# Optimization experiments

Hardware: AMD Instinct MI355X
Metric: run time of the kernel (lower is better)

The kernel has to match this reference:

```python
import jax, jax.numpy as jnp
import numpy as np

B, N, E = 64, 256, 2048          # graphs per batch, nodes per subgraph, edges per subgraph
V, D, H = 50000, 128, 4          # vocab_size, hidden_dim, heads
NEG_SLOPE = 0.2                  # PyG GATConv default LeakyReLU slope


def setup_inputs() -> dict:
    key = jax.random.key(0)
    ks = jax.random.split(key, 16)
    s = 0.05
    return {
        "neighbors_node1": jax.random.randint(ks[0], (B, N), 0, V),
        "neighbors_node2": jax.random.randint(ks[1], (B, N), 0, V),
        "adj1": jax.random.randint(ks[2], (B, 2, E), 0, N),
        "adj2": jax.random.randint(ks[3], (B, 2, E), 0, N),
        "emb": jax.random.normal(ks[4], (V + 1, D), jnp.float32) * 0.02,
        # GATConv 1: lin weight [H*D, D], att_src/att_dst [H, D], bias [D] (concat=False)
        "W1": jax.random.normal(ks[5], (H * D, D), jnp.float32) * s,
        "att_src1": jax.random.normal(ks[6], (H, D), jnp.float32) * s,
        "att_dst1": jax.random.normal(ks[7], (H, D), jnp.float32) * s,
        "b1": jnp.zeros((D,), jnp.float32),
        # GATConv 2
        "W2": jax.random.normal(ks[8], (H * D, D), jnp.float32) * s,
        "att_src2": jax.random.normal(ks[9], (H, D), jnp.float32) * s,
        "att_dst2": jax.random.normal(ks[10], (H, D), jnp.float32) * s,
        "b2": jnp.zeros((D,), jnp.float32),
        # final MLP: Linear(2D -> 1)
        "mlp_w": jax.random.normal(ks[11], (1, 2 * D), jnp.float32) * s,
        "mlp_b": jnp.zeros((1,), jnp.float32),
    }


def _gat_conv(x, edge_index, W, a_src, a_dst, bias):
    """PyG GATConv, concat=False (mean over heads), with self-loops.
    x: [N, D] node features; edge_index: [2, E] (row=src j, col=dst i)."""
    xh = (x @ W.T).reshape(N, H, D)                      # [N, H, D]
    loop = jnp.arange(N)
    src = jnp.concatenate([edge_index[0], loop])          # [E+N]
    dst = jnp.concatenate([edge_index[1], loop])
    asrc = jnp.einsum('nhd,hd->nh', xh, a_src)            # [N, H]
    adst = jnp.einsum('nhd,hd->nh', xh, a_dst)
    e = jax.nn.leaky_relu(asrc[src] + adst[dst], NEG_SLOPE)   # [E+N, H]
    # softmax over incoming edges of each dst node
    m = jax.ops.segment_max(e, dst, num_segments=N)
    ex = jnp.exp(e - m[dst])
    denom = jax.ops.segment_sum(ex, dst, num_segments=N)
    alpha = ex / denom[dst]                               # [E+N, H]
    out = jax.ops.segment_sum(xh[src] * alpha[:, :, None], dst, num_segments=N)  # [N, H, D]
    return out.mean(axis=1) + bias                        # [N, D]


def reference(neighbors_node1, neighbors_node2, adj1, adj2, emb,
              W1, att_src1, att_dst1, b1,
              W2, att_src2, att_dst2, b2,
              mlp_w, mlp_b):
    f1 = jax.vmap(lambda n, ei: _gat_conv(emb[n], ei, W1, att_src1, att_dst1, b1))(
        neighbors_node1, adj1)                            # [B, N, D]
    f2 = jax.vmap(lambda n, ei: _gat_conv(emb[n], ei, W2, att_src2, att_dst2, b2))(
        neighbors_node2, adj2)
    feats = jnp.concatenate([f1[:, 0], f2[:, 0]], axis=-1)  # center node of each subgraph -> [B, 2D]
    return (feats @ mlp_w.T + mlp_b)[:, 0]                # [B]
```

## Files before the change

### kernel.cpp

```cpp
#include <hip/hip_runtime.h>
#include <hip/hip_bf16.h>

#define Bg 64
#define Nn 256
#define Ee 2048
#define Dd 128
#define Hh 4
#define MAXJ 40
#define RS 132
#define MAGIC 0x9E3779B1u

__device__ __forceinline__ float bf2f(unsigned short u) {
    return __uint_as_float(((unsigned)u) << 16);
}

__global__ __launch_bounds__(512) void gat_fused_kernel(
    const int* nn1, const int* nn2, const int* adj1, const int* adj2,
    const void* emb,
    const void* W1, const void* as1, const void* ad1, const void* b1,
    const void* W2, const void* as2, const void* ad2, const void* b2,
    const void* mlpw, const void* mlpb,
    float* wv, int f32arg, void* out)
{
    __shared__ float s_wv[24 * RS];
    __shared__ float s_rows[2 * MAXJ * RS];
    __shared__ int   s_nodes[2][Nn];
    __shared__ int   s_srcj[2][MAXJ];
    __shared__ int   s_gid[2 * MAXJ];
    __shared__ int   s_cnt[2];
    __shared__ int   s_f32;
    __shared__ float s_ps[2 * MAXJ * Hh], s_pm[2 * MAXJ * Hh];
    __shared__ float s_pd[2 * Hh], s_hval[2 * Hh], s_bdot[2];
    __shared__ float s_red[2];

    const int tid = threadIdx.x;
    const int x = blockIdx.x;

    if (x < 8) {
        const int l = x >> 2, h = x & 3;
        float* s_av   = s_wv;
        float* s_part = s_rows;

        int f32 = f32arg;
        if (f32 < 0) {
            if (tid < 64) {
                float v = bf2f(((const unsigned short*)W1)[tid]);
                unsigned long long m = __ballot(!(v > -64.f && v < 64.f));
                if (tid == 0) s_f32 = (m != 0ull) ? 1 : 0;
            }
            __syncthreads();
            f32 = s_f32;
        }

        if (tid < 384) {
            int t = tid >> 7, d = tid & 127;
            const void* p; long off;
            if (t == 0)      { p = l ? as2 : as1; off = (long)h * Dd + d; }
            else if (t == 1) { p = l ? ad2 : ad1; off = (long)h * Dd + d; }
            else             { p = mlpw;          off = (long)l * Dd + d; }
            s_av[tid] = f32 ? ((const float*)p)[off]
                            : bf2f(((const unsigned short*)p)[off]);
        }
        __syncthreads();

        {
            const int kc = (tid & 31) * 4;
            const int dg = tid >> 5;
            const int d0 = dg * 8;
            float acc[3][4] = {};
            if (f32) {
                const float* Wf = (const float*)(l ? W2 : W1) + (long)h * Dd * Dd;
                #pragma unroll
                for (int dd = 0; dd < 8; ++dd) {
                    int d = d0 + dd;
                    float4 w = *(const float4*)(Wf + (long)d * Dd + kc);
                    #pragma unroll
                    for (int t = 0; t < 3; ++t) {
                        float a = s_av[t * Dd + d];
                        acc[t][0] += a * w.x; acc[t][1] += a * w.y;
                        acc[t][2] += a * w.z; acc[t][3] += a * w.w;
                    }
                }
            } else {
                const unsigned short* Wb =
                    (const unsigned short*)(l ? W2 : W1) + (long)h * Dd * Dd;
                #pragma unroll
                for (int dd = 0; dd < 8; ++dd) {
                    int d = d0 + dd;
                    ushort4 u = *(const ushort4*)(Wb + (long)d * Dd + kc);
                    float wx = bf2f(u.x), wy = bf2f(u.y);
                    float wz = bf2f(u.z), ww = bf2f(u.w);
                    #pragma unroll
                    for (int t = 0; t < 3; ++t) {
                        float a = s_av[t * Dd + d];
                        acc[t][0] += a * wx; acc[t][1] += a * wy;
                        acc[t][2] += a * wz; acc[t][3] += a * ww;
                    }
                }
            }
            const int dg2 = tid >> 5;
            #pragma unroll
            for (int t = 0; t < 3; ++t)
                *(float4*)&s_part[(dg2 * 3 + t) * Dd + kc] =
                    make_float4(acc[t][0], acc[t][1], acc[t][2], acc[t][3]);
        }
        __syncthreads();

        if (tid < 384) {
            int t = tid >> 7, k = tid & 127;
            float s = 0.f;
            #pragma unroll
            for (int g = 0; g < 16; ++g) s += s_part[(g * 3 + t) * Dd + k];
            wv[((l * 3 + t) * 4 + h) * Dd + k] = s;
        }

        if (h == 0) {
            float p = 0.f;
            if (tid < 128) {
                const void* bias = l ? b2 : b1;
                float bv = f32 ? ((const float*)bias)[tid]
                               : bf2f(((const unsigned short*)bias)[tid]);
                p = bv * s_av[2 * Dd + tid];
            }
            #pragma unroll
            for (int off = 32; off > 0; off >>= 1) p += __shfl_down(p, off);
            if (tid == 0 || tid == 64) s_red[tid >> 6] = p;
            __syncthreads();
            if (tid == 0) {
                float a = s_red[0] + s_red[1];
                if (l == 0) a += f32 ? ((const float*)mlpb)[0]
                                     : bf2f(((const unsigned short*)mlpb)[0]);
                wv[3072 + l] = a;
            }
        }

        __threadfence();
        __syncthreads();
        if (tid == 0)
            atomicExch((unsigned*)wv + 3080 + x, MAGIC);
        return;
    }

    const int b = x - 8;

    const int* adjp0 = adj1 + (long)b * 2 * Ee;
    const int* adjp1 = adj2 + (long)b * 2 * Ee;
    int4 d0 = ((const int4*)(adjp0 + Ee))[tid];
    int4 s0 = ((const int4*)adjp0)[tid];
    int4 d1 = ((const int4*)(adjp1 + Ee))[tid];
    int4 s1 = ((const int4*)adjp1)[tid];

    {
        int l = tid >> 8, n = tid & 255;
        s_nodes[l][n] = (l ? nn2 : nn1)[b * Nn + n];
    }
    if (tid < 2) s_cnt[tid] = 0;

    int f32 = f32arg;
    if (f32 < 0 && tid < 64) {
        float v = bf2f(((const unsigned short*)W1)[tid]);
        unsigned long long m = __ballot(!(v > -64.f && v < 64.f));
        if (tid == 0) s_f32 = (m != 0ull) ? 1 : 0;
    }
    __syncthreads();
    if (f32 < 0) f32 = s_f32;

    {
        #define SCAN1(c, sv, l) \
            if ((c) == 0) { int p = atomicAdd(&s_cnt[l], 1); \
                            if (p < MAXJ - 1) s_srcj[l][p] = (sv); }
        SCAN1(d0.x, s0.x, 0) SCAN1(d0.y, s0.y, 0)
        SCAN1(d0.z, s0.z, 0) SCAN1(d0.w, s0.w, 0)
        SCAN1(d1.x, s1.x, 1) SCAN1(d1.y, s1.y, 1)
        SCAN1(d1.z, s1.z, 1) SCAN1(d1.w, s1.w, 1)
        #undef SCAN1
    }
    __syncthreads();

    int c0 = s_cnt[0]; if (c0 > MAXJ - 1) c0 = MAXJ - 1; c0 += 1;
    int c1 = s_cnt[1]; if (c1 > MAXJ - 1) c1 = MAXJ - 1; c1 += 1;
    const int tot = c0 + c1;

    if (tid < 2 * MAXJ) {
        int l = tid >= MAXJ;
        int j = l ? tid - MAXJ : tid;
        int cl = l ? c1 : c0;
        int base = l ? c0 : 0;
        if (j < cl) {
            int src = (j == cl - 1) ? 0 : s_srcj[l][j];
            s_gid[base + j] = s_nodes[l][src];
        }
    }
    __syncthreads();

    if (f32) {
        for (int idx = tid; idx < tot * 32; idx += 512) {
            int j = idx >> 5, k4 = (idx & 31) << 2;
            long gid = s_gid[j];
            float4 f = ((const float4*)emb)[gid * 32 + (k4 >> 2)];
            *(float4*)&s_rows[j * RS + k4] = f;
        }
    } else {
        for (int idx = tid; idx < tot * 16; idx += 512) {
            int j = idx >> 4, k8 = (idx & 15) << 3;
            long gid = s_gid[j];
            uint4 u = *(const uint4*)((const unsigned short*)emb + gid * Dd + k8);
            float4 f0 = make_float4(bf2f(u.x & 0xffff), bf2f(u.x >> 16),
                                    bf2f(u.y & 0xffff), bf2f(u.y >> 16));
            float4 f1 = make_float4(bf2f(u.z & 0xffff), bf2f(u.z >> 16),
                                    bf2f(u.w & 0xffff), bf2f(u.w >> 16));
            *(float4*)&s_rows[j * RS + k8] = f0;
            *(float4*)&s_rows[j * RS + k8 + 4] = f1;
        }
    }

    if (tid < 8) {
        unsigned* fl = (unsigned*)wv + 3080 + tid;
        while (atomicAdd(fl, 0u) != MAGIC) __builtin_amdgcn_s_sleep(2);
    }
    __syncthreads();
    __threadfence();

    for (int i = tid; i < 768; i += 512) {
        float4 f = ((const float4*)wv)[i];
        int el = i * 4, row = el >> 7, k = el & 127;
        *(float4*)&s_wv[row * RS + k] = f;
    }
    if (tid < 2) s_bdot[tid] = wv[3072 + tid];
    __syncthreads();

    const int ntask = tot * 8 + 8;
    for (int task = tid; task < ntask; task += 512) {
        int j, h, t, l;
        if (task < tot * 8) {
            j = task >> 3; h = (task >> 1) & 3; t = (task & 1) ? 2 : 0;
            l = (j < c0) ? 0 : 1;
        } else {
            int z = task - tot * 8;
            l = z >> 2; h = z & 3; t = 1;
            j = l ? (tot - 1) : (c0 - 1);
        }
        const float4* r4 = (const float4*)(s_rows + j * RS);
        const float4* w4 = (const float4*)(s_wv + ((l * 3 + t) * Hh + h) * RS);
        float acc = 0.f;
        #pragma unroll 8
        for (int k = 0; k < 32; ++k) {
            float4 a = r4[k], w = w4[k];
            acc += a.x * w.x + a.y * w.y + a.z * w.z + a.w * w.w;
        }
        if (task < tot * 8) {
            if (task & 1) s_pm[j * Hh + h] = acc;
            else          s_ps[j * Hh + h] = acc;
        } else {
            s_pd[(l << 2) | h] = acc;
        }
    }
    __syncthreads();

    {
        const int w = tid >> 6, lane = tid & 63;
        const int l = w >> 2, h = w & 3;
        const int j0 = l ? c0 : 0;
        const int cntl = (l ? tot : c0) - j0;
        const float pd = s_pd[w];
        const bool valid = lane < cntl;
        const int j = j0 + (valid ? lane : 0);
        float e = valid ? (s_ps[j * Hh + h] + pd) : -1e30f;
        e = (e >= 0.f) ? e : 0.2f * e;
        float m = e;
        #pragma unroll
        for (int off = 32; off > 0; off >>= 1)
            m = fmaxf(m, __shfl_xor(m, off));
        float ex = valid ? expf(e - m) : 0.f;
        float pm = valid ? s_pm[j * Hh + h] : 0.f;
        float den = ex, num = ex * pm;
        #pragma unroll
        for (int off = 32; off > 0; off >>= 1) {
            den += __shfl_xor(den, off);
            num += __shfl_xor(num, off);
        }
        if (lane == 0) s_hval[w] = num / den;
    }
    __syncthreads();

    if (tid == 0) {
        float r = 0.25f * (s_hval[0] + s_hval[1] + s_hval[2] + s_hval[3]) + s_bdot[0]
                + 0.25f * (s_hval[4] + s_hval[5] + s_hval[6] + s_hval[7]) + s_bdot[1];
        if (f32) ((float*)out)[b] = r;
        else     ((__hip_bfloat16*)out)[b] = __float2bfloat16(r);
    }
}

extern "C" void kernel_launch(void* const* d_in, const int* in_sizes, int n_in,
                              void* d_out, int out_size, void* d_ws, size_t ws_size,
                              hipStream_t stream) {
    float* wv = (float*)d_ws;

    int sz5 = (in_sizes && n_in > 5) ? in_sizes[5] : 0;
    int f32arg = (sz5 == 512 * 128 * 4) ? 1 : ((sz5 == 512 * 128 * 2) ? 0 : -1);

    gat_fused_kernel<<<8 + Bg, 512, 0, stream>>>(
        (const int*)d_in[0],
        (const int*)d_in[1],
        (const int*)d_in[2],
        (const int*)d_in[3],
        d_in[4],
        d_in[5],   d_in[6],   d_in[7],
        d_in[8],
        d_in[9],   d_in[10],  d_in[11],
        d_in[12],
        d_in[13],  d_in[14],
        wv, f32arg, d_out);
}
```

Before: 111.5 us.

## Replicate weight-vector precompute per block, drop inter-block flag wait

```diff
diff --git a/kernel.cpp b/kernel.cpp
--- a/kernel.cpp
+++ b/kernel.cpp
@@ -8,7 +8,6 @@
 #define Hh 4
 #define MAXJ 40
 #define RS 132
-#define MAGIC 0x9E3779B1u
 
 __device__ __forceinline__ float bf2f(unsigned short u) {
     return __uint_as_float(((unsigned)u) << 16);
@@ -19,129 +18,22 @@
     const void* emb,
     const void* W1, const void* as1, const void* ad1, const void* b1,
     const void* W2, const void* as2, const void* ad2, const void* b2,
-    const void* mlpw, const void* mlpb,
-    float* wv, int f32arg, void* out)
+    const void* mlpw, const void* mlpb, int f32arg, void* out)
 {
     __shared__ float s_wv[24 * RS];
     __shared__ float s_rows[2 * MAXJ * RS];
+    __shared__ float s_att[2304];
     __shared__ int   s_nodes[2][Nn];
     __shared__ int   s_srcj[2][MAXJ];
     __shared__ int   s_gid[2 * MAXJ];
     __shared__ int   s_cnt[2];
     __shared__ int   s_f32;
     __shared__ float s_ps[2 * MAXJ * Hh], s_pm[2 * MAXJ * Hh];
-    __shared__ float s_pd[2 * Hh], s_hval[2 * Hh], s_bdot[2];
-    __shared__ float s_red[2];
+    __shared__ float s_pd[8], s_hval[8];
+    __shared__ float s_red[4];
 
     const int tid = threadIdx.x;
-    const int x = blockIdx.x;
-
-    if (x < 8) {
-        const int l = x >> 2, h = x & 3;
-        float* s_av   = s_wv;
-        float* s_part = s_rows;
-
-        int f32 = f32arg;
-        if (f32 < 0) {
-            if (tid < 64) {
-                float v = bf2f(((const unsigned short*)W1)[tid]);
-                unsigned long long m = __ballot(!(v > -64.f && v < 64.f));
-                if (tid == 0) s_f32 = (m != 0ull) ? 1 : 0;
-            }
-            __syncthreads();
-            f32 = s_f32;
-        }
-
-        if (tid < 384) {
-            int t = tid >> 7, d = tid & 127;
-            const void* p; long off;
-            if (t == 0)      { p = l ? as2 : as1; off = (long)h * Dd + d; }
-            else if (t == 1) { p = l ? ad2 : ad1; off = (long)h * Dd + d; }
-            else             { p = mlpw;          off = (long)l * Dd + d; }
-            s_av[tid] = f32 ? ((const float*)p)[off]
-                            : bf2f(((const unsigned short*)p)[off]);
-        }
-        __syncthreads();
-
-        {
-            const int kc = (tid & 31) * 4;
-            const int dg = tid >> 5;
-            const int d0 = dg * 8;
-            float acc[3][4] = {};
-            if (f32) {
-                const float* Wf = (const float*)(l ? W2 : W1) + (long)h * Dd * Dd;
-                #pragma unroll
-                for (int dd = 0; dd < 8; ++dd) {
-                    int d = d0 + dd;
-                    float4 w = *(const float4*)(Wf + (long)d * Dd + kc);
-                    #pragma unroll
-                    for (int t = 0; t < 3; ++t) {
-                        float a = s_av[t * Dd + d];
-                        acc[t][0] += a * w.x; acc[t][1] += a * w.y;
-                        acc[t][2] += a * w.z; acc[t][3] += a * w.w;
-                    }
-                }
-            } else {
-                const unsigned short* Wb =
-                    (const unsigned short*)(l ? W2 : W1) + (long)h * Dd * Dd;
-                #pragma unroll
-                for (int dd = 0; dd < 8; ++dd) {
-                    int d = d0 + dd;
-                    ushort4 u = *(const ushort4*)(Wb + (long)d * Dd + kc);
-                    float wx = bf2f(u.x), wy = bf2f(u.y);
-                    float wz = bf2f(u.z), ww = bf2f(u.w);
-                    #pragma unroll
-                    for (int t = 0; t < 3; ++t) {
-                        float a = s_av[t * Dd + d];
-                        acc[t][0] += a * wx; acc[t][1] += a * wy;
-                        acc[t][2] += a * wz; acc[t][3] += a * ww;
-                    }
-                }
-            }
-            const int dg2 = tid >> 5;
-            #pragma unroll
-            for (int t = 0; t < 3; ++t)
-                *(float4*)&s_part[(dg2 * 3 + t) * Dd + kc] =
-                    make_float4(acc[t][0], acc[t][1], acc[t][2], acc[t][3]);
-        }
-        __syncthreads();
-
-        if (tid < 384) {
-            int t = tid >> 7, k = tid & 127;
-            float s = 0.f;
-            #pragma unroll
-            for (int g = 0; g < 16; ++g) s += s_part[(g * 3 + t) * Dd + k];
-            wv[((l * 3 + t) * 4 + h) * Dd + k] = s;
-        }
-
-        if (h == 0) {
-            float p = 0.f;
-            if (tid < 128) {
-                const void* bias = l ? b2 : b1;
-                float bv = f32 ? ((const float*)bias)[tid]
-                               : bf2f(((const unsigned short*)bias)[tid]);
-                p = bv * s_av[2 * Dd + tid];
-            }
-            #pragma unroll
-            for (int off = 32; off > 0; off >>= 1) p += __shfl_down(p, off);
-            if (tid == 0 || tid == 64) s_red[tid >> 6] = p;
-            __syncthreads();
-            if (tid == 0) {
-                float a = s_red[0] + s_red[1];
-                if (l == 0) a += f32 ? ((const float*)mlpb)[0]
-                                     : bf2f(((const unsigned short*)mlpb)[0]);
-                wv[3072 + l] = a;
-            }
-        }
-
-        __threadfence();
-        __syncthreads();
-        if (tid == 0)
-            atomicExch((unsigned*)wv + 3080 + x, MAGIC);
-        return;
-    }
-
-    const int b = x - 8;
+    const int b = blockIdx.x;
 
     const int* adjp0 = adj1 + (long)b * 2 * Ee;
     const int* adjp1 = adj2 + (long)b * 2 * Ee;
@@ -157,13 +49,61 @@
     if (tid < 2) s_cnt[tid] = 0;
 
     int f32 = f32arg;
-    if (f32 < 0 && tid < 64) {
-        float v = bf2f(((const unsigned short*)W1)[tid]);
-        unsigned long long m = __ballot(!(v > -64.f && v < 64.f));
-        if (tid == 0) s_f32 = (m != 0ull) ? 1 : 0;
-    }
-    __syncthreads();
-    if (f32 < 0) f32 = s_f32;
+    if (f32 < 0) {
+        if (tid < 64) {
+            float v = bf2f(((const unsigned short*)W1)[tid]);
+            unsigned long long m = __ballot(!(v > -64.f && v < 64.f));
+            if (tid == 0) s_f32 = (m != 0ull) ? 1 : 0;
+        }
+        __syncthreads();
+        f32 = s_f32;
+    }
+
+    if (f32) {
+        for (int i = tid; i < 576; i += 512) {
+            int e = i * 4;
+            const float* p; int dst;
+            if (e < 2048) {
+                int l = e >> 10, t = (e >> 9) & 1, h = (e >> 7) & 3, d = e & 127;
+                p = (const float*)(l ? (t ? ad2 : as2) : (t ? ad1 : as1)) + h * Dd + d;
+                dst = ((l * 2 + t) * 4 + h) * Dd + d;
+            } else {
+                p = (const float*)mlpw + (e - 2048);
+                dst = e;
+            }
+            *(float4*)&s_att[dst] = *(const float4*)p;
+        }
+    } else {
+        if (tid < 288) {
+            int e = tid * 8;
+            const unsigned short* p; int dst;
+            if (e < 2048) {
+                int l = e >> 10, t = (e >> 9) & 1, h = (e >> 7) & 3, d = e & 127;
+                p = (const unsigned short*)(l ? (t ? ad2 : as2) : (t ? ad1 : as1)) + h * Dd + d;
+                dst = ((l * 2 + t) * 4 + h) * Dd + d;
+            } else {
+                p = (const unsigned short*)mlpw + (e - 2048);
+                dst = e;
+            }
+            uint4 u = *(const uint4*)p;
+            *(float4*)&s_att[dst] = make_float4(bf2f(u.x & 0xffff), bf2f(u.x >> 16),
+                                                bf2f(u.y & 0xffff), bf2f(u.y >> 16));
+            *(float4*)&s_att[dst + 4] = make_float4(bf2f(u.z & 0xffff), bf2f(u.z >> 16),
+                                                    bf2f(u.w & 0xffff), bf2f(u.w >> 16));
+        }
+    }
+
+    float bv = 0.f;
+    if (tid < 256) {
+        int l = tid >> 7, d = tid & 127;
+        const void* bp = l ? b2 : b1;
+        bv = f32 ? ((const float*)bp)[d] : bf2f(((const unsigned short*)bp)[d]);
+    }
+    float mb = 0.f;
+    if (tid == 0)
+        mb = f32 ? ((const float*)mlpb)[0] : bf2f(((const unsigned short*)mlpb)[0]);
+
+    __syncthreads();
 
     {
         #define SCAN1(c, sv, l) \
@@ -193,40 +133,146 @@
     }
     __syncthreads();
 
+    const int na = f32 ? tot * 32 : tot * 16;
+    float4 ga, gb; uint4 ua;
+    bool va = false, vb = false;
     if (f32) {
-        for (int idx = tid; idx < tot * 32; idx += 512) {
+        if (tid < na) {
+            int j = tid >> 5, k4 = (tid & 31) << 2;
+            ga = ((const float4*)emb)[(long)s_gid[j] * 32 + (k4 >> 2)];
+            va = true;
+        }
+        int t2 = tid + 512;
+        if (t2 < na) {
+            int j = t2 >> 5, k4 = (t2 & 31) << 2;
+            gb = ((const float4*)emb)[(long)s_gid[j] * 32 + (k4 >> 2)];
+            vb = true;
+        }
+    } else {
+        if (tid < na) {
+            int j = tid >> 4, k8 = (tid & 15) << 3;
+            ua = *(const uint4*)((const unsigned short*)emb + (long)s_gid[j] * Dd + k8);
+            va = true;
+        }
+    }
+
+    {
+        const int w = tid >> 6, lane = tid & 63;
+        const int l = w >> 2, h = w & 3;
+        const float* a0 = s_att + ((l * 2 + 0) * 4 + h) * Dd;
+        const float* a1 = s_att + ((l * 2 + 1) * 4 + h) * Dd;
+        const float* a2 = s_att + 2048 + l * Dd;
+        if (f32) {
+            const int k0 = (lane & 31) * 4;
+            const int d0f = (lane >> 5) * 64;
+            const float* Wf = (const float*)(l ? W2 : W1) + h * Dd * Dd;
+            float acc[3][4] = {};
+            #pragma unroll 8
+            for (int i = 0; i < 64; ++i) {
+                int d = d0f + i;
+                float4 wr = *(const float4*)(Wf + d * Dd + k0);
+                float x0 = a0[d], x1 = a1[d], x2 = a2[d];
+                acc[0][0] += x0 * wr.x; acc[0][1] += x0 * wr.y;
+                acc[0][2] += x0 * wr.z; acc[0][3] += x0 * wr.w;
+                acc[1][0] += x1 * wr.x; acc[1][1] += x1 * wr.y;
+                acc[1][2] += x1 * wr.z; acc[1][3] += x1 * wr.w;
+                acc[2][0] += x2 * wr.x; acc[2][1] += x2 * wr.y;
+                acc[2][2] += x2 * wr.z; acc[2][3] += x2 * wr.w;
+            }
+            #pragma unroll
+            for (int t = 0; t < 3; ++t)
+                #pragma unroll
+                for (int c = 0; c < 4; ++c)
+                    acc[t][c] += __shfl_xor(acc[t][c], 32);
+            if (lane < 32) {
+                #pragma unroll
+                for (int t = 0; t < 3; ++t)
+                    *(float4*)&s_wv[((l * 3 + t) * 4 + h) * RS + k0] =
+                        make_float4(acc[t][0], acc[t][1], acc[t][2], acc[t][3]);
+            }
+        } else {
+            const int k0 = (lane & 15) * 8;
+            const int d0b = (lane >> 4) * 32;
+            const unsigned short* Wb =
+                (const unsigned short*)(l ? W2 : W1) + h * Dd * Dd;
+            float acc[3][8] = {};
+            #pragma unroll 4
+            for (int i = 0; i < 32; ++i) {
+                int d = d0b + i;
+                uint4 u = *(const uint4*)(Wb + d * Dd + k0);
+                float wc[8] = { bf2f(u.x & 0xffff), bf2f(u.x >> 16),
+                                bf2f(u.y & 0xffff), bf2f(u.y >> 16),
+                                bf2f(u.z & 0xffff), bf2f(u.z >> 16),
+                                bf2f(u.w & 0xffff), bf2f(u.w >> 16) };
+                float x0 = a0[d], x1 = a1[d], x2 = a2[d];
+                #pragma unroll
+                for (int c = 0; c < 8; ++c) {
+                    acc[0][c] += x0 * wc[c];
+                    acc[1][c] += x1 * wc[c];
+                    acc[2][c] += x2 * wc[c];
+                }
+            }
+            #pragma unroll
+            for (int t = 0; t < 3; ++t)
+                #pragma unroll
+                for (int c = 0; c < 8; ++c) {
+                    acc[t][c] += __shfl_xor(acc[t][c], 16);
+                    acc[t][c] += __shfl_xor(acc[t][c], 32);
+                }
+            if (lane < 16) {
+                #pragma unroll
+                for (int t = 0; t < 3; ++t) {
+                    *(float4*)&s_wv[((l * 3 + t) * 4 + h) * RS + k0] =
+                        make_float4(acc[t][0], acc[t][1], acc[t][2], acc[t][3]);
+                    *(float4*)&s_wv[((l * 3 + t) * 4 + h) * RS + k0 + 4] =
+                        make_float4(acc[t][4], acc[t][5], acc[t][6], acc[t][7]);
+                }
+            }
+        }
+    }
+
+    {
+        float p = (tid < 256) ? bv * s_att[2048 + ((tid >> 7) * Dd) + (tid & 127)] : 0.f;
+        #pragma unroll
+        for (int off = 32; off > 0; off >>= 1) p += __shfl_down(p, off);
+        if (tid < 256 && (tid & 63) == 0) s_red[tid >> 6] = p;
+    }
+
+    if (f32) {
+        if (va) {
+            int j = tid >> 5, k4 = (tid & 31) << 2;
+            *(float4*)&s_rows[j * RS + k4] = ga;
+        }
+        if (vb) {
+            int t2 = tid + 512, j = t2 >> 5, k4 = (t2 & 31) << 2;
+            *(float4*)&s_rows[j * RS + k4] = gb;
+        }
+        for (int idx = tid + 1024; idx < na; idx += 512) {
             int j = idx >> 5, k4 = (idx & 31) << 2;
-            long gid = s_gid[j];
-            float4 f = ((const float4*)emb)[gid * 32 + (k4 >> 2)];
-            *(float4*)&s_rows[j * RS + k4] = f;
+            *(float4*)&s_rows[j * RS + k4] =
+                ((const float4*)emb)[(long)s_gid[j] * 32 + (k4 >> 2)];
         }
     } else {
-        for (int idx = tid; idx < tot * 16; idx += 512) {
+        if (va) {
+            int j = tid >> 4, k8 = (tid & 15) << 3;
+            *(float4*)&s_rows[j * RS + k8] =
+                make_float4(bf2f(ua.x & 0xffff), bf2f(ua.x >> 16),
+                            bf2f(ua.y & 0xffff), bf2f(ua.y >> 16));
+            *(float4*)&s_rows[j * RS + k8 + 4] =
+                make_float4(bf2f(ua.z & 0xffff), bf2f(ua.z >> 16),
+                            bf2f(ua.w & 0xffff), bf2f(ua.w >> 16));
+        }
+        for (int idx = tid + 512; idx < na; idx += 512) {
             int j = idx >> 4, k8 = (idx & 15) << 3;
-            long gid = s_gid[j];
-            uint4 u = *(const uint4*)((const unsigned short*)emb + gid * Dd + k8);
-            float4 f0 = make_float4(bf2f(u.x & 0xffff), bf2f(u.x >> 16),
-                                    bf2f(u.y & 0xffff), bf2f(u.y >> 16));
-            float4 f1 = make_float4(bf2f(u.z & 0xffff), bf2f(u.z >> 16),
-                                    bf2f(u.w & 0xffff), bf2f(u.w >> 16));
-            *(float4*)&s_rows[j * RS + k8] = f0;
-            *(float4*)&s_rows[j * RS + k8 + 4] = f1;
-        }
-    }
-
-    if (tid < 8) {
-        unsigned* fl = (unsigned*)wv + 3080 + tid;
-        while (atomicAdd(fl, 0u) != MAGIC) __builtin_amdgcn_s_sleep(2);
-    }
-    __syncthreads();
-    __threadfence();
-
-    for (int i = tid; i < 768; i += 512) {
-        float4 f = ((const float4*)wv)[i];
-        int el = i * 4, row = el >> 7, k = el & 127;
-        *(float4*)&s_wv[row * RS + k] = f;
-    }
-    if (tid < 2) s_bdot[tid] = wv[3072 + tid];
+            uint4 u = *(const uint4*)((const unsigned short*)emb + (long)s_gid[j] * Dd + k8);
+            *(float4*)&s_rows[j * RS + k8] =
+                make_float4(bf2f(u.x & 0xffff), bf2f(u.x >> 16),
+                            bf2f(u.y & 0xffff), bf2f(u.y >> 16));
+            *(float4*)&s_rows[j * RS + k8 + 4] =
+                make_float4(bf2f(u.z & 0xffff), bf2f(u.z >> 16),
+                            bf2f(u.w & 0xffff), bf2f(u.w >> 16));
+        }
+    }
     __syncthreads();
 
     const int ntask = tot * 8 + 8;
@@ -284,8 +330,10 @@
     __syncthreads();
 
     if (tid == 0) {
-        float r = 0.25f * (s_hval[0] + s_hval[1] + s_hval[2] + s_hval[3]) + s_bdot[0]
-                + 0.25f * (s_hval[4] + s_hval[5] + s_hval[6] + s_hval[7]) + s_bdot[1];
+        float bd0 = s_red[0] + s_red[1] + mb;
+        float bd1 = s_red[2] + s_red[3];
+        float r = 0.25f * (s_hval[0] + s_hval[1] + s_hval[2] + s_hval[3]) + bd0
+                + 0.25f * (s_hval[4] + s_hval[5] + s_hval[6] + s_hval[7]) + bd1;
         if (f32) ((float*)out)[b] = r;
         else     ((__hip_bfloat16*)out)[b] = __float2bfloat16(r);
     }
@@ -294,12 +342,10 @@
 extern "C" void kernel_launch(void* const* d_in, const int* in_sizes, int n_in,
                               void* d_out, int out_size, void* d_ws, size_t ws_size,
                               hipStream_t stream) {
-    float* wv = (float*)d_ws;
-
     int sz5 = (in_sizes && n_in > 5) ? in_sizes[5] : 0;
     int f32arg = (sz5 == 512 * 128 * 4) ? 1 : ((sz5 == 512 * 128 * 2) ? 0 : -1);
 
-    gat_fused_kernel<<<8 + Bg, 512, 0, stream>>>(
+    gat_fused_kernel<<<Bg, 512, 0, stream>>>(
         (const int*)d_in[0],
         (const int*)d_in[1],
         (const int*)d_in[2],
@@ -310,5 +356,5 @@
         d_in[9],   d_in[10],  d_in[11],
         d_in[12],
         d_in[13],  d_in[14],
-        wv, f32arg, d_out);
+        f32arg, d_out);
 }
```

After: 106.2 us. -4.8%, faster.
